# Optimization experiments

Measured on AMD Instinct MI355X. Metric: run time of the kernel, lower is better.

Reference implementation:

```python
import jax, jax.numpy as jnp
import numpy as np

EPS = 1e-10

def setup_inputs() -> dict:
    key = jax.random.key(0)
    kq, kk, kv = jax.random.split(key, 3)
    B, S, D = 8, 4096, 64
    q = jax.random.normal(kq, (B, S, D), dtype=jnp.float32)
    k = jax.random.normal(kk, (B, S, D), dtype=jnp.float32)
    v = jax.random.normal(kv, (B, S, D), dtype=jnp.float32)
    attention_mask = jnp.zeros((B, S, S), dtype=bool)
    return {"q": q, "k": k, "v": v, "attention_mask": attention_mask}

def reference(q, k, v, attention_mask):
    # L2-normalize q and k along feature dim (norm + eps in denominator, per torch code)
    q = q / (jnp.linalg.norm(q, axis=-1, keepdims=True) + EPS)
    k = k / (jnp.linalg.norm(k, axis=-1, keepdims=True) + EPS)
    # [B, S, S] cosine similarity scores
    scores = jnp.einsum('bqd,bkd->bqk', q, k)
    scores = jnp.where(attention_mask, -jnp.inf, scores)
    soft_attention = jax.nn.softmax(scores, axis=-1)
    # dropout_rate = 0.0 -> identity
    output = jnp.einsum('bqk,bkd->bqd', soft_attention, v)
    return (output, soft_attention)
```

## Files before the change

### kernel.cpp

```cpp
#include <hip/hip_runtime.h>
#include <math.h>

#define BB 8
#define SS 4096
#define DD 64
#define NT (SS / 64)

typedef float  f32x4 __attribute__((ext_vector_type(4)));
typedef short  s16x4 __attribute__((ext_vector_type(4)));
typedef short  s16x8 __attribute__((ext_vector_type(8)));
typedef unsigned char u8x16 __attribute__((ext_vector_type(16)));

__device__ __forceinline__ short f2bf(float f) {
  unsigned u = __builtin_bit_cast(unsigned, f);
  u += 0x7FFFu + ((u >> 16) & 1u);
  return (short)(u >> 16);
}

__global__ __launch_bounds__(256) void k_norm(const float* __restrict__ q,
                                              const float* __restrict__ k,
                                              short* __restrict__ qn,
                                              short* __restrict__ kn) {
  const long BS = (long)BB * SS;
  long row = (long)blockIdx.x * 4 + (threadIdx.x >> 6);
  int lane = threadIdx.x & 63;
  const float* src;
  short* dst;
  if (row < BS) { src = q + row * DD; dst = qn + row * DD; }
  else          { src = k + (row - BS) * DD; dst = kn + (row - BS) * DD; }
  float x = src[lane];
  float ss = x * x;
#pragma unroll
  for (int m = 32; m >= 1; m >>= 1) ss += __shfl_xor(ss, m);
  float inv = 1.0f / (sqrtf(ss) + 1e-10f);
  dst[lane] = f2bf(x * inv);
}

__global__ __launch_bounds__(256) void k_vtrans(const float* __restrict__ v,
                                                short* __restrict__ vt) {
  __shared__ short tile[64][65];
  int b = blockIdx.y;
  int s0 = blockIdx.x * 64;
  const float* V = v + ((long)b * SS + s0) * DD;
  int t = threadIdx.x;
#pragma unroll
  for (int i = 0; i < 16; i++) {
    int flat = t + 256 * i;
    int sl = flat >> 6, d = flat & 63;
    tile[sl][d] = f2bf(V[flat]);
  }
  __syncthreads();
  short* VT = vt + (long)b * DD * SS + s0;
#pragma unroll
  for (int i = 0; i < 16; i++) {
    int flat = t + 256 * i;
    int d = flat >> 6, sl = flat & 63;
    VT[(long)d * SS + sl] = tile[sl][d];
  }
}

__global__ __launch_bounds__(256) void k_fused(const short* __restrict__ qn,
                                               const short* __restrict__ kn,
                                               const short* __restrict__ vt,
                                               const unsigned char* __restrict__ mask,
                                               float* __restrict__ O,
                                               float* __restrict__ P) {
  __shared__ __align__(16) short Kt[2][4096];
  __shared__ __align__(16) short Vt[2][4096];
  __shared__ __align__(16) unsigned long long bitsL[NT * 64];
  unsigned short* bits16 = (unsigned short*)bitsL;

  int b = blockIdx.x & 7;
  int q0 = (blockIdx.x >> 3) << 6;
  int wid = threadIdx.x >> 6, lane = threadIdx.x & 63;
  int l15 = lane & 15, g = lane >> 4;
  int qr = q0 + (wid << 4);

  const short* Qr = qn + ((long)(b * SS) + qr + l15) * DD;
  s16x8 qf0 = *(const s16x8*)(Qr + 8 * g);
  s16x8 qf1 = *(const s16x8*)(Qr + 32 + 8 * g);

  const short* Kb = kn + (long)b * SS * DD;
  const short* Vb = vt + (long)b * DD * SS;

  int sr = lane >> 3, sc = lane & 7;
  int r0 = (wid << 4) + sr, r1 = r0 + 8;
  const short* Ksrc0 = Kb + (long)r0 * DD + sc * 8;
  const short* Ksrc1 = Kb + (long)r1 * DD + sc * 8;
  const short* Vsrc0 = Vb + (long)r0 * SS + sc * 8;
  const short* Vsrc1 = Vb + (long)r1 * SS + sc * 8;
  int sd0 = r0 * DD + ((sc ^ sr) << 3);
  int sd1 = r1 * DD + ((sc ^ sr) << 3);
  int swk = l15 & 7;

  int mrow = (wid << 4) + (lane >> 2);
  int mpiece = lane & 3;
  const unsigned char* Msrc = mask + ((long)(b * SS) + q0 + mrow) * SS + mpiece * 16;

  u8x16 mCur = __builtin_nontemporal_load((const u8x16*)Msrc);
  u8x16 mNext = __builtin_nontemporal_load((const u8x16*)(Msrc + 64));
  s16x8 kst0 = *(const s16x8*)Ksrc0;
  s16x8 kst1 = *(const s16x8*)Ksrc1;
  {
    unsigned bv = 0;
#pragma unroll
    for (int i = 0; i < 16; i++) bv |= (mCur[i] ? 1u : 0u) << i;
    bits16[(0 * 64 + mrow) * 4 + mpiece] = (unsigned short)bv;
  }
  *(s16x8*)&Kt[0][sd0] = kst0;
  *(s16x8*)&Kt[0][sd1] = kst1;
  __syncthreads();

  float acc = 0.f;
  int cur = 0;
  for (int t = 0; t < NT; ++t) {
    if (t + 1 < NT) {
      long koff = (long)(t + 1) * 64 * DD;
      kst0 = *(const s16x8*)(Ksrc0 + koff);
      kst1 = *(const s16x8*)(Ksrc1 + koff);
    }
    u8x16 mFar = mNext;
    if (t + 2 < NT)
      mFar = __builtin_nontemporal_load((const u8x16*)(Msrc + (long)(t + 2) * 64));
    if (t + 1 < NT) {
      unsigned bv = 0;
#pragma unroll
      for (int i = 0; i < 16; i++) bv |= (mNext[i] ? 1u : 0u) << i;
      bits16[((t + 1) * 64 + mrow) * 4 + mpiece] = (unsigned short)bv;
    }
    unsigned long long w64 = bitsL[t * 64 + (wid << 4) + l15];
    const short* Kc = &Kt[cur][0];
#pragma unroll
    for (int tt = 0; tt < 4; ++tt) {
      const short* krow = Kc + ((tt << 4) + l15) * DD;
      s16x8 a0 = *(const s16x8*)(krow + ((g ^ swk) << 3));
      s16x8 a1 = *(const s16x8*)(krow + (((4 + g) ^ swk) << 3));
      f32x4 c = {0.f, 0.f, 0.f, 0.f};
      c = __builtin_amdgcn_mfma_f32_16x16x32_bf16(a0, qf0, c, 0, 0, 0);
      c = __builtin_amdgcn_mfma_f32_16x16x32_bf16(a1, qf1, c, 0, 0, 0);
#pragma unroll
      for (int r = 0; r < 4; ++r) {
        unsigned bit = (unsigned)(w64 >> ((tt << 4) + (g << 2) + r)) & 1u;
        acc += bit ? 0.f : __expf(c[r]);
      }
    }
    if (t + 1 < NT) {
      short* Kd = &Kt[cur ^ 1][0];
      *(s16x8*)(Kd + sd0) = kst0;
      *(s16x8*)(Kd + sd1) = kst1;
    }
    __syncthreads();
    cur ^= 1;
    mNext = mFar;
  }
  acc += __shfl_xor(acc, 16);
  acc += __shfl_xor(acc, 32);
  float linv = -__logf(acc);

  kst0 = *(const s16x8*)Ksrc0;
  kst1 = *(const s16x8*)Ksrc1;
  s16x8 vst0 = *(const s16x8*)Vsrc0;
  s16x8 vst1 = *(const s16x8*)Vsrc1;
  *(s16x8*)&Kt[0][sd0] = kst0;
  *(s16x8*)&Kt[0][sd1] = kst1;
  *(s16x8*)&Vt[0][sd0] = vst0;
  *(s16x8*)&Vt[0][sd1] = vst1;
  __syncthreads();

  float* Prow = P + ((long)(b * SS) + qr + l15) * SS;
  f32x4 o0 = {0, 0, 0, 0}, o1 = {0, 0, 0, 0}, o2 = {0, 0, 0, 0}, o3 = {0, 0, 0, 0};
  cur = 0;
  for (int t = 0; t < NT; ++t) {
    if (t + 1 < NT) {
      long koff = (long)(t + 1) * 64 * DD;
      kst0 = *(const s16x8*)(Ksrc0 + koff);
      kst1 = *(const s16x8*)(Ksrc1 + koff);
      vst0 = *(const s16x8*)(Vsrc0 + (t + 1) * 64);
      vst1 = *(const s16x8*)(Vsrc1 + (t + 1) * 64);
    }
    unsigned long long w64 = bitsL[t * 64 + (wid << 4) + l15];
    const short* Kc = &Kt[cur][0];
    const short* Vc = &Vt[cur][0];

    f32x4 p[4];
#pragma unroll
    for (int tt = 0; tt < 4; ++tt) {
      const short* krow = Kc + ((tt << 4) + l15) * DD;
      s16x8 a0 = *(const s16x8*)(krow + ((g ^ swk) << 3));
      s16x8 a1 = *(const s16x8*)(krow + (((4 + g) ^ swk) << 3));
      f32x4 c = {0.f, 0.f, 0.f, 0.f};
      c = __builtin_amdgcn_mfma_f32_16x16x32_bf16(a0, qf0, c, 0, 0, 0);
      c = __builtin_amdgcn_mfma_f32_16x16x32_bf16(a1, qf1, c, 0, 0, 0);
#pragma unroll
      for (int r = 0; r < 4; ++r) {
        unsigned bit = (unsigned)(w64 >> ((tt << 4) + (g << 2) + r)) & 1u;
        p[tt][r] = bit ? 0.f : __expf(c[r] + linv);
      }
      __builtin_nontemporal_store(p[tt],
          (f32x4*)(Prow + (t << 6) + (tt << 4) + (g << 2)));
    }

    s16x8 pa0, pa1;
#pragma unroll
    for (int j = 0; j < 4; ++j) {
      pa0[j] = f2bf(p[0][j]); pa0[4 + j] = f2bf(p[1][j]);
      pa1[j] = f2bf(p[2][j]); pa1[4 + j] = f2bf(p[3][j]);
    }

#pragma unroll
    for (int n = 0; n < 4; ++n) {
      const short* vrow = Vc + ((n << 4) + l15) * DD;
      int g2 = g >> 1, hh = (g & 1) << 2;
      s16x4 lo0 = *(const s16x4*)(vrow + (((g2    ) ^ swk) << 3) + hh);
      s16x4 hi0 = *(const s16x4*)(vrow + (((g2 + 2) ^ swk) << 3) + hh);
      s16x4 lo1 = *(const s16x4*)(vrow + (((g2 + 4) ^ swk) << 3) + hh);
      s16x4 hi1 = *(const s16x4*)(vrow + (((g2 + 6) ^ swk) << 3) + hh);
      s16x8 vf0 = __builtin_shufflevector(lo0, hi0, 0, 1, 2, 3, 4, 5, 6, 7);
      s16x8 vf1 = __builtin_shufflevector(lo1, hi1, 0, 1, 2, 3, 4, 5, 6, 7);
      f32x4* on = (n == 0) ? &o0 : (n == 1) ? &o1 : (n == 2) ? &o2 : &o3;
      *on = __builtin_amdgcn_mfma_f32_16x16x32_bf16(pa0, vf0, *on, 0, 0, 0);
      *on = __builtin_amdgcn_mfma_f32_16x16x32_bf16(pa1, vf1, *on, 0, 0, 0);
    }

    if (t + 1 < NT) {
      short* Kd = &Kt[cur ^ 1][0];
      short* Vd = &Vt[cur ^ 1][0];
      *(s16x8*)(Kd + sd0) = kst0;
      *(s16x8*)(Kd + sd1) = kst1;
      *(s16x8*)(Vd + sd0) = vst0;
      *(s16x8*)(Vd + sd1) = vst1;
    }
    __syncthreads();
    cur ^= 1;
  }

  float* Ob = O + ((long)(b * SS) + qr) * DD;
#pragma unroll
  for (int r = 0; r < 4; ++r) {
    int row = (g << 2) + r;
    Ob[row * DD +  0 + l15] = o0[r];
    Ob[row * DD + 16 + l15] = o1[r];
    Ob[row * DD + 32 + l15] = o2[r];
    Ob[row * DD + 48 + l15] = o3[r];
  }
}

extern "C" void kernel_launch(void* const* d_in, const int* in_sizes, int n_in,
                              void* d_out, int out_size, void* d_ws, size_t ws_size,
                              hipStream_t stream) {
  const float* q = (const float*)d_in[0];
  const float* k = (const float*)d_in[1];
  const float* v = (const float*)d_in[2];
  const unsigned char* mask = (const unsigned char*)d_in[3];

  const long BSD = (long)BB * SS * DD;
  short* qn = (short*)d_ws;
  short* kn = qn + BSD;
  short* vtp = kn + BSD;

  float* O = (float*)d_out;
  float* P = O + BSD;

  k_norm<<<dim3(2 * BB * SS / 4), dim3(256), 0, stream>>>(q, k, qn, kn);
  k_vtrans<<<dim3(SS / 64, BB), dim3(256), 0, stream>>>(v, vtp);
  k_fused<<<dim3(BB * SS / 64), dim3(256), 0, stream>>>(qn, kn, vtp, mask, O, P);
}
```

Before: 309.0 us.

## Split fused attention into rowsum and attention kernels with key-dimension halves

Splits the single fused kernel into two kernels, a row-sum pass and a probability/output pass. Each kernel processes half of the key dimension per block, which doubles the grid (1024 blocks). Row sums are combined with atomics into a global buffer, and output partials are combined with float atomics into a zeroed O. Mask bits are written to a global workspace instead of shared memory. This adds parallelism and removes the large per-block shared bit buffer, which may raise occupancy. The cost is extra launches and memsets, atomic traffic, global bitmask writes and reads, and nondeterministic summation order.

```diff
diff --git a/kernel.cpp b/kernel.cpp
--- a/kernel.cpp
+++ b/kernel.cpp
@@ -4,7 +4,7 @@
 #define BB 8
 #define SS 4096
 #define DD 64
-#define NT (SS / 64)
+#define NTH 32
 
 typedef float  f32x4 __attribute__((ext_vector_type(4)));
 typedef short  s16x4 __attribute__((ext_vector_type(4)));
@@ -59,19 +59,17 @@
   }
 }
 
-__global__ __launch_bounds__(256) void k_fused(const short* __restrict__ qn,
-                                               const short* __restrict__ kn,
-                                               const short* __restrict__ vt,
-                                               const unsigned char* __restrict__ mask,
-                                               float* __restrict__ O,
-                                               float* __restrict__ P) {
+__global__ __launch_bounds__(256) void k_rowsum(const short* __restrict__ qn,
+                                                const short* __restrict__ kn,
+                                                const unsigned char* __restrict__ mask,
+                                                unsigned short* __restrict__ bits16,
+                                                float* __restrict__ accG) {
   __shared__ __align__(16) short Kt[2][4096];
-  __shared__ __align__(16) short Vt[2][4096];
-  __shared__ __align__(16) unsigned long long bitsL[NT * 64];
-  unsigned short* bits16 = (unsigned short*)bitsL;
-
+  __shared__ __align__(16) unsigned long long bitsT[2][64];
   int b = blockIdx.x & 7;
-  int q0 = (blockIdx.x >> 3) << 6;
+  int half = (blockIdx.x >> 3) & 1;
+  int q0 = (blockIdx.x >> 4) << 6;
+  int t0 = half * NTH;
   int wid = threadIdx.x >> 6, lane = threadIdx.x & 63;
   int l15 = lane & 15, g = lane >> 4;
   int qr = q0 + (wid << 4);
@@ -80,8 +78,112 @@
   s16x8 qf0 = *(const s16x8*)(Qr + 8 * g);
   s16x8 qf1 = *(const s16x8*)(Qr + 32 + 8 * g);
 
-  const short* Kb = kn + (long)b * SS * DD;
-  const short* Vb = vt + (long)b * DD * SS;
+  const short* Kb = kn + (long)b * SS * DD + (long)t0 * 64 * DD;
+
+  int sr = lane >> 3, sc = lane & 7;
+  int r0 = (wid << 4) + sr, r1 = r0 + 8;
+  const short* Ksrc0 = Kb + (long)r0 * DD + sc * 8;
+  const short* Ksrc1 = Kb + (long)r1 * DD + sc * 8;
+  int sd0 = r0 * DD + ((sc ^ sr) << 3);
+  int sd1 = r1 * DD + ((sc ^ sr) << 3);
+  int swk = l15 & 7;
+
+  int mrow = (wid << 4) + (lane >> 2);
+  int mpiece = lane & 3;
+  const unsigned char* Msrc = mask + ((long)(b * SS) + q0 + mrow) * SS + t0 * 64 + mpiece * 16;
+  unsigned short* Bdst = bits16 + ((long)(b * SS) + q0 + mrow) * (SS / 16) + mpiece;
+  unsigned short* bT16 = (unsigned short*)bitsT;
+
+  u8x16 mCur = __builtin_nontemporal_load((const u8x16*)Msrc);
+  u8x16 mNext = __builtin_nontemporal_load((const u8x16*)(Msrc + 64));
+  s16x8 kst0 = *(const s16x8*)Ksrc0;
+  s16x8 kst1 = *(const s16x8*)Ksrc1;
+  {
+    unsigned bv = 0;
+#pragma unroll
+    for (int i = 0; i < 16; i++) bv |= (mCur[i] ? 1u : 0u) << i;
+    bT16[(0 * 64 + mrow) * 4 + mpiece] = (unsigned short)bv;
+    __builtin_nontemporal_store((unsigned short)bv, Bdst + (long)(t0) * 4);
+  }
+  *(s16x8*)&Kt[0][sd0] = kst0;
+  *(s16x8*)&Kt[0][sd1] = kst1;
+  __syncthreads();
+
+  float acc = 0.f;
+  int cur = 0;
+  for (int t = 0; t < NTH; ++t) {
+    if (t + 1 < NTH) {
+      long koff = (long)(t + 1) * 64 * DD;
+      kst0 = *(const s16x8*)(Ksrc0 + koff);
+      kst1 = *(const s16x8*)(Ksrc1 + koff);
+    }
+    u8x16 mFar = mNext;
+    if (t + 2 < NTH)
+      mFar = __builtin_nontemporal_load((const u8x16*)(Msrc + (long)(t + 2) * 64));
+    if (t + 1 < NTH) {
+      unsigned bv = 0;
+#pragma unroll
+      for (int i = 0; i < 16; i++) bv |= (mNext[i] ? 1u : 0u) << i;
+      bT16[((cur ^ 1) * 64 + mrow) * 4 + mpiece] = (unsigned short)bv;
+      __builtin_nontemporal_store((unsigned short)bv, Bdst + (long)(t0 + t + 1) * 4);
+    }
+    unsigned long long w64 = bitsT[cur][(wid << 4) + l15];
+    const short* Kc = &Kt[cur][0];
+#pragma unroll
+    for (int tt = 0; tt < 4; ++tt) {
+      const short* krow = Kc + ((tt << 4) + l15) * DD;
+      s16x8 a0 = *(const s16x8*)(krow + ((g ^ swk) << 3));
+      s16x8 a1 = *(const s16x8*)(krow + (((4 + g) ^ swk) << 3));
+      f32x4 c = {0.f, 0.f, 0.f, 0.f};
+      c = __builtin_amdgcn_mfma_f32_16x16x32_bf16(a0, qf0, c, 0, 0, 0);
+      c = __builtin_amdgcn_mfma_f32_16x16x32_bf16(a1, qf1, c, 0, 0, 0);
+#pragma unroll
+      for (int r = 0; r < 4; ++r) {
+        unsigned bit = (unsigned)(w64 >> ((tt << 4) + (g << 2) + r)) & 1u;
+        acc += bit ? 0.f : __expf(c[r]);
+      }
+    }
+    if (t + 1 < NTH) {
+      short* Kd = &Kt[cur ^ 1][0];
+      *(s16x8*)(Kd + sd0) = kst0;
+      *(s16x8*)(Kd + sd1) = kst1;
+    }
+    __syncthreads();
+    cur ^= 1;
+    mNext = mFar;
+  }
+  acc += __shfl_xor(acc, 16);
+  acc += __shfl_xor(acc, 32);
+  if (lane < 16) atomicAdd(&accG[(long)b * SS + qr + l15], acc);
+}
+
+__global__ __launch_bounds__(256) void k_attn(const short* __restrict__ qn,
+                                              const short* __restrict__ kn,
+                                              const short* __restrict__ vt,
+                                              const unsigned short* __restrict__ bits16,
+                                              const float* __restrict__ accG,
+                                              float* __restrict__ O,
+                                              float* __restrict__ P) {
+  __shared__ __align__(16) short Kt[2][4096];
+  __shared__ __align__(16) short Vt[2][4096];
+  int b = blockIdx.x & 7;
+  int half = (blockIdx.x >> 3) & 1;
+  int q0 = (blockIdx.x >> 4) << 6;
+  int t0 = half * NTH;
+  int wid = threadIdx.x >> 6, lane = threadIdx.x & 63;
+  int l15 = lane & 15, g = lane >> 4;
+  int qr = q0 + (wid << 4);
+
+  const short* Qr = qn + ((long)(b * SS) + qr + l15) * DD;
+  s16x8 qf0 = *(const s16x8*)(Qr + 8 * g);
+  s16x8 qf1 = *(const s16x8*)(Qr + 32 + 8 * g);
+
+  const short* Kb = kn + (long)b * SS * DD + (long)t0 * 64 * DD;
+  const short* Vb = vt + (long)b * DD * SS + t0 * 64;
+  const unsigned long long* B64 =
+      (const unsigned long long*)bits16 + ((long)(b * SS) + qr + l15) * (SS / 64);
+  float linv = -__logf(accG[(long)b * SS + qr + l15]);
+  float* Prow = P + ((long)(b * SS) + qr + l15) * SS;
 
   int sr = lane >> 3, sc = lane & 7;
   int r0 = (wid << 4) + sr, r1 = r0 + 8;
@@ -93,43 +195,31 @@
   int sd1 = r1 * DD + ((sc ^ sr) << 3);
   int swk = l15 & 7;
 
-  int mrow = (wid << 4) + (lane >> 2);
-  int mpiece = lane & 3;
-  const unsigned char* Msrc = mask + ((long)(b * SS) + q0 + mrow) * SS + mpiece * 16;
-
-  u8x16 mCur = __builtin_nontemporal_load((const u8x16*)Msrc);
-  u8x16 mNext = __builtin_nontemporal_load((const u8x16*)(Msrc + 64));
   s16x8 kst0 = *(const s16x8*)Ksrc0;
   s16x8 kst1 = *(const s16x8*)Ksrc1;
-  {
-    unsigned bv = 0;
-#pragma unroll
-    for (int i = 0; i < 16; i++) bv |= (mCur[i] ? 1u : 0u) << i;
-    bits16[(0 * 64 + mrow) * 4 + mpiece] = (unsigned short)bv;
-  }
+  s16x8 vst0 = *(const s16x8*)Vsrc0;
+  s16x8 vst1 = *(const s16x8*)Vsrc1;
   *(s16x8*)&Kt[0][sd0] = kst0;
   *(s16x8*)&Kt[0][sd1] = kst1;
+  *(s16x8*)&Vt[0][sd0] = vst0;
+  *(s16x8*)&Vt[0][sd1] = vst1;
   __syncthreads();
 
-  float acc = 0.f;
+  f32x4 o0 = {0, 0, 0, 0}, o1 = {0, 0, 0, 0}, o2 = {0, 0, 0, 0}, o3 = {0, 0, 0, 0};
   int cur = 0;
-  for (int t = 0; t < NT; ++t) {
-    if (t + 1 < NT) {
+  for (int t = 0; t < NTH; ++t) {
+    if (t + 1 < NTH) {
       long koff = (long)(t + 1) * 64 * DD;
       kst0 = *(const s16x8*)(Ksrc0 + koff);
       kst1 = *(const s16x8*)(Ksrc1 + koff);
-    }
-    u8x16 mFar = mNext;
-    if (t + 2 < NT)
-      mFar = __builtin_nontemporal_load((const u8x16*)(Msrc + (long)(t + 2) * 64));
-    if (t + 1 < NT) {
-      unsigned bv = 0;
-#pragma unroll
-      for (int i = 0; i < 16; i++) bv |= (mNext[i] ? 1u : 0u) << i;
-      bits16[((t + 1) * 64 + mrow) * 4 + mpiece] = (unsigned short)bv;
-    }
-    unsigned long long w64 = bitsL[t * 64 + (wid << 4) + l15];
+      vst0 = *(const s16x8*)(Vsrc0 + (t + 1) * 64);
+      vst1 = *(const s16x8*)(Vsrc1 + (t + 1) * 64);
+    }
+    unsigned long long w64 = B64[t0 + t];
     const short* Kc = &Kt[cur][0];
+    const short* Vc = &Vt[cur][0];
+
+    f32x4 p[4];
 #pragma unroll
     for (int tt = 0; tt < 4; ++tt) {
       const short* krow = Kc + ((tt << 4) + l15) * DD;
@@ -141,63 +231,10 @@
 #pragma unroll
       for (int r = 0; r < 4; ++r) {
         unsigned bit = (unsigned)(w64 >> ((tt << 4) + (g << 2) + r)) & 1u;
-        acc += bit ? 0.f : __expf(c[r]);
-      }
-    }
-    if (t + 1 < NT) {
-      short* Kd = &Kt[cur ^ 1][0];
-      *(s16x8*)(Kd + sd0) = kst0;
-      *(s16x8*)(Kd + sd1) = kst1;
-    }
-    __syncthreads();
-    cur ^= 1;
-    mNext = mFar;
-  }
-  acc += __shfl_xor(acc, 16);
-  acc += __shfl_xor(acc, 32);
-  float linv = -__logf(acc);
-
-  kst0 = *(const s16x8*)Ksrc0;
-  kst1 = *(const s16x8*)Ksrc1;
-  s16x8 vst0 = *(const s16x8*)Vsrc0;
-  s16x8 vst1 = *(const s16x8*)Vsrc1;
-  *(s16x8*)&Kt[0][sd0] = kst0;
-  *(s16x8*)&Kt[0][sd1] = kst1;
-  *(s16x8*)&Vt[0][sd0] = vst0;
-  *(s16x8*)&Vt[0][sd1] = vst1;
-  __syncthreads();
-
-  float* Prow = P + ((long)(b * SS) + qr + l15) * SS;
-  f32x4 o0 = {0, 0, 0, 0}, o1 = {0, 0, 0, 0}, o2 = {0, 0, 0, 0}, o3 = {0, 0, 0, 0};
-  cur = 0;
-  for (int t = 0; t < NT; ++t) {
-    if (t + 1 < NT) {
-      long koff = (long)(t + 1) * 64 * DD;
-      kst0 = *(const s16x8*)(Ksrc0 + koff);
-      kst1 = *(const s16x8*)(Ksrc1 + koff);
-      vst0 = *(const s16x8*)(Vsrc0 + (t + 1) * 64);
-      vst1 = *(const s16x8*)(Vsrc1 + (t + 1) * 64);
-    }
-    unsigned long long w64 = bitsL[t * 64 + (wid << 4) + l15];
-    const short* Kc = &Kt[cur][0];
-    const short* Vc = &Vt[cur][0];
-
-    f32x4 p[4];
-#pragma unroll
-    for (int tt = 0; tt < 4; ++tt) {
-      const short* krow = Kc + ((tt << 4) + l15) * DD;
-      s16x8 a0 = *(const s16x8*)(krow + ((g ^ swk) << 3));
-      s16x8 a1 = *(const s16x8*)(krow + (((4 + g) ^ swk) << 3));
-      f32x4 c = {0.f, 0.f, 0.f, 0.f};
-      c = __builtin_amdgcn_mfma_f32_16x16x32_bf16(a0, qf0, c, 0, 0, 0);
-      c = __builtin_amdgcn_mfma_f32_16x16x32_bf16(a1, qf1, c, 0, 0, 0);
-#pragma unroll
-      for (int r = 0; r < 4; ++r) {
-        unsigned bit = (unsigned)(w64 >> ((tt << 4) + (g << 2) + r)) & 1u;
         p[tt][r] = bit ? 0.f : __expf(c[r] + linv);
       }
       __builtin_nontemporal_store(p[tt],
-          (f32x4*)(Prow + (t << 6) + (tt << 4) + (g << 2)));
+          (f32x4*)(Prow + ((t0 + t) << 6) + (tt << 4) + (g << 2)));
     }
 
     s16x8 pa0, pa1;
@@ -222,7 +259,7 @@
       *on = __builtin_amdgcn_mfma_f32_16x16x32_bf16(pa1, vf1, *on, 0, 0, 0);
     }
 
-    if (t + 1 < NT) {
+    if (t + 1 < NTH) {
       short* Kd = &Kt[cur ^ 1][0];
       short* Vd = &Vt[cur ^ 1][0];
       *(s16x8*)(Kd + sd0) = kst0;
@@ -238,10 +275,10 @@
 #pragma unroll
   for (int r = 0; r < 4; ++r) {
     int row = (g << 2) + r;
-    Ob[row * DD +  0 + l15] = o0[r];
-    Ob[row * DD + 16 + l15] = o1[r];
-    Ob[row * DD + 32 + l15] = o2[r];
-    Ob[row * DD + 48 + l15] = o3[r];
+    atomicAdd(&Ob[row * DD +  0 + l15], o0[r]);
+    atomicAdd(&Ob[row * DD + 16 + l15], o1[r]);
+    atomicAdd(&Ob[row * DD + 32 + l15], o2[r]);
+    atomicAdd(&Ob[row * DD + 48 + l15], o3[r]);
   }
 }
 
@@ -257,11 +294,17 @@
   short* qn = (short*)d_ws;
   short* kn = qn + BSD;
   short* vtp = kn + BSD;
+  unsigned short* bits = (unsigned short*)(vtp + BSD);
+  float* accG = (float*)(bits + (long)BB * SS * (SS / 16));
 
   float* O = (float*)d_out;
   float* P = O + BSD;
 
+  hipMemsetAsync(accG, 0, (size_t)BB * SS * sizeof(float), stream);
+  hipMemsetAsync(O, 0, (size_t)BSD * sizeof(float), stream);
+
   k_norm<<<dim3(2 * BB * SS / 4), dim3(256), 0, stream>>>(q, k, qn, kn);
   k_vtrans<<<dim3(SS / 64, BB), dim3(256), 0, stream>>>(v, vtp);
-  k_fused<<<dim3(BB * SS / 64), dim3(256), 0, stream>>>(qn, kn, vtp, mask, O, P);
-}
+  k_rowsum<<<dim3(2 * BB * SS / 64), dim3(256), 0, stream>>>(qn, kn, mask, bits, accG);
+  k_attn<<<dim3(2 * BB * SS / 64), dim3(256), 0, stream>>>(qn, kn, vtp, bits, accG, O, P);
+}
```

After: 311.5 us. About the same (+0.8%).
